# Performance work log

Measured on AMD Instinct MI355X. Metric: run time of the kernel, lower is better.

The kernel has to match this reference:

```python
import jax, jax.numpy as jnp
import numpy as np

S, H, A = 16384, 1024, 1024


def setup_inputs() -> dict:
    key = jax.random.key(0)
    k1, k2, k3, k4, k5, k6 = jax.random.split(key, 6)
    enc_out = jax.random.normal(k1, (S, 1, H), dtype=jnp.float32)
    dec_h = jax.random.normal(k2, (1, H), dtype=jnp.float32)
    mask = jax.random.randint(k3, (S, 1), 0, 2) == 1  # bool [S,1]
    # learned params (torch Linear stores weight as [out, in]; y = x @ W.T)
    W2_dec = jax.random.normal(k4, (A, H), dtype=jnp.float32) * 0.02
    W1_enc = jax.random.normal(k5, (A, H), dtype=jnp.float32) * 0.02
    V = jax.random.normal(k6, (1, A), dtype=jnp.float32) * 0.02
    return {"enc_out": enc_out, "dec_h": dec_h, "mask": mask,
            "W2_dec": W2_dec, "W1_enc": W1_enc, "V": V}


def reference(enc_out, dec_h, mask, W2_dec, W1_enc, V):
    enc = jnp.squeeze(enc_out, axis=1)            # [S, H]
    d = dec_h @ W2_dec.T                          # [1, A]
    e = enc @ W1_enc.T                            # [S, A]
    u = jnp.tanh(d + e) @ V.T                     # [S, 1]
    u = jnp.where(mask, -jnp.inf, u)              # masked logits (returned, like in-place fill)
    a = jax.nn.softmax(u, axis=0)                 # softmax over seq dim
    out = jnp.sum(a * enc, axis=0)                # [H]
    return (out, u)
```

## Files before the change

### kernel.cpp

```cpp
#include <hip/hip_runtime.h>
#include <math.h>
#include <stdint.h>

#define S_DIM 16384
#define H_DIM 1024
#define A_DIM 1024

#define MASK_NEG (-3.0e38f)

typedef __attribute__((ext_vector_type(8))) _Float16 f16x8;
typedef __attribute__((ext_vector_type(4))) float f32x4;
typedef __attribute__((address_space(3))) uint32_t as3_u32;
typedef __attribute__((address_space(1))) uint32_t as1_u32;

__device__ __forceinline__ float fast_tanh(float x) {
    float e = __expf(2.0f * x);
    return 1.0f - 2.0f * __builtin_amdgcn_rcpf(e + 1.0f);
}


__global__ __launch_bounds__(256) void prep_kernel(
        const float* __restrict__ W1, _Float16* __restrict__ W1_h,
        const float* __restrict__ dec_h, const float* __restrict__ W2,
        float* __restrict__ d, float* __restrict__ u_acc,
        const void* __restrict__ mask, int* __restrict__ mflag) {
    const int b = blockIdx.x;
    const int t = threadIdx.x;
    if (b < 64) {
        const int tb = b >> 4, kt = b & 15;
        uint4* dchunk = (uint4*)W1_h + (size_t)(tb * 16 + kt) * 1024;
        const float* srow = W1 + (size_t)tb * 256 * H_DIM + kt * 32;
        #pragma unroll
        for (int it = 0; it < 4; ++it) {
            const int idx  = it * 256 + t;
            const int r    = idx >> 2;
            const int slot = idx & 3;
            const int cg   = (slot + (r >> 1)) & 3;
            const float* sp = srow + (size_t)r * H_DIM + cg * 8;
            float4 v0 = ((const float4*)sp)[0];
            float4 v1 = ((const float4*)sp)[1];
            union { _Float16 h[8]; uint4 u; } pk;
            pk.h[0] = (_Float16)v0.x; pk.h[1] = (_Float16)v0.y;
            pk.h[2] = (_Float16)v0.z; pk.h[3] = (_Float16)v0.w;
            pk.h[4] = (_Float16)v1.x; pk.h[5] = (_Float16)v1.y;
            pk.h[6] = (_Float16)v1.z; pk.h[7] = (_Float16)v1.w;
            dchunk[idx] = pk.u;
        }
        u_acc[b * 256 + t] = 0.0f;
    } else if (b < 1088) {
        const int a = b - 64;
        const float* row = W2 + (size_t)a * H_DIM;
        float s = 0.0f;
        for (int h = t; h < H_DIM; h += 256) s += dec_h[h] * row[h];
        #pragma unroll
        for (int off = 32; off; off >>= 1) s += __shfl_down(s, off, 64);
        __shared__ float wsum[4];
        if ((t & 63) == 0) wsum[t >> 6] = s;
        __syncthreads();
        if (t == 0) d[a] = wsum[0] + wsum[1] + wsum[2] + wsum[3];
    } else {
        const unsigned char* mb = (const unsigned char*)mask;
        unsigned int orv = 0;
        for (int i = t; i < S_DIM; i += 256)
            if (i & 3) orv |= mb[i];
        __shared__ int oflag;
        if (t == 0) oflag = 0;
        __syncthreads();
        if (orv) oflag = 1;
        __syncthreads();
        if (t == 0) mflag[0] = oflag;
    }
}

__global__ __launch_bounds__(512, 1) void fused_gemm_f16_2ph(
        const float* __restrict__ enc,
        const _Float16* __restrict__ Bg,
        const float* __restrict__ V,
        const float* __restrict__ d,
        float* __restrict__ u_acc) {
    __shared__ __align__(16) _Float16 AB[2][32768];

    const int tid  = threadIdx.x;
    const int wave = tid >> 6;
    const int lane = tid & 63;
    const int quad = lane >> 4;
    const int l16  = lane & 15;
    const int wm   = wave >> 2;
    const int wn   = wave & 3;
    const int s0   = blockIdx.x * 256;
    const int a0   = blockIdx.y * 256;

    const int rowoff = (wave & 3) * 64;
    const int lrow  = lane >> 2;
    const int slotc = lane & 3;
    const int cg    = (slotc + (lrow >> 1)) & 3;

    const float* asrc[4];
    #pragma unroll
    for (int j = 0; j < 4; ++j)
        asrc[j] = enc + (size_t)(s0 + rowoff + j * 16 + lrow) * H_DIM + cg * 8;
    const _Float16* gtile = Bg + (size_t)blockIdx.y * (16 * 8192) + rowoff * 32 + lane * 8;
    _Float16* lbaseB = &AB[0][8192 + rowoff * 32];

    const int sw = ((quad - (l16 >> 1)) & 3) * 8;
    int aoff[8], boff[4];
    #pragma unroll
    for (int mi = 0; mi < 8; ++mi)
        aoff[mi] = (wm * 128 + mi * 16 + l16) * 32 + sw;
    #pragma unroll
    for (int ni = 0; ni < 4; ++ni)
        boff[ni] = 8192 + (wn * 64 + ni * 16 + l16) * 32 + sw;

    f32x4 acc[8][4];
    #pragma unroll
    for (int mi = 0; mi < 8; ++mi)
        #pragma unroll
        for (int ni = 0; ni < 4; ++ni)
            acc[mi][ni] = (f32x4){0.f, 0.f, 0.f, 0.f};

    const _Float16* hAB = &AB[0][0];

    auto pack8 = [](float4 a, float4 b) -> uint4 {
        union { _Float16 h[8]; uint4 u; } pk;
        pk.h[0] = (_Float16)a.x; pk.h[1] = (_Float16)a.y;
        pk.h[2] = (_Float16)a.z; pk.h[3] = (_Float16)a.w;
        pk.h[4] = (_Float16)b.x; pk.h[5] = (_Float16)b.y;
        pk.h[6] = (_Float16)b.z; pk.h[7] = (_Float16)b.w;
        return pk.u;
    };
    auto STAGE_A = [&](int buf, int s, int kt) {
        #pragma unroll
        for (int j = 0; j < 4; ++j) {
            float4 x0 = *(const float4*)(asrc[j] + kt * 32);
            float4 x1 = *(const float4*)(asrc[j] + kt * 32 + 4);
            *(uint4*)&AB[buf][s * 16384 + rowoff * 32 + j * 512 + lane * 8] = pack8(x0, x1);
        }
    };
    auto COMPUTE = [&](int base) {
        f16x8 bf[4];
        #pragma unroll
        for (int ni = 0; ni < 4; ++ni)
            bf[ni] = *(const f16x8*)&hAB[base + boff[ni]];
        #pragma unroll
        for (int mi = 0; mi < 8; ++mi) {
            f16x8 af = *(const f16x8*)&hAB[base + aoff[mi]];
            #pragma unroll
            for (int ni = 0; ni < 4; ++ni)
                acc[mi][ni] = __builtin_amdgcn_mfma_f32_16x16x32_f16(af, bf[ni], acc[mi][ni], 0, 0, 0);
        }
    };

    if (wave < 4) {
        STAGE_A(0, 0, 0);
        STAGE_A(0, 1, 1);
        asm volatile("s_waitcnt lgkmcnt(0)" ::: "memory");
    } else {
        #pragma unroll
        for (int s = 0; s < 2; ++s)
            #pragma unroll
            for (int j = 0; j < 4; ++j)
                __builtin_amdgcn_global_load_lds(
                    (const as1_u32*)(const void*)(gtile + s * 8192 + j * 512),
                    (as3_u32*)(void*)(lbaseB + s * 16384 + j * 512), 16, 0, 0);
    }

    for (int ph = 0; ph < 16; ++ph) {
        const int b = ph & 1;
        if (wave >= 4) {
            if (ph < 15) {
                #pragma unroll
                for (int s = 0; s < 2; ++s)
                    #pragma unroll
                    for (int j = 0; j < 4; ++j)
                        __builtin_amdgcn_global_load_lds(
                            (const as1_u32*)(const void*)(gtile + (size_t)((ph + 1) * 2 + s) * 8192 + j * 512),
                            (as3_u32*)(void*)(lbaseB + (b ^ 1) * 32768 + s * 16384 + j * 512),
                            16, 0, 0);
                asm volatile("s_waitcnt vmcnt(8)" ::: "memory");
            } else {
                asm volatile("s_waitcnt vmcnt(0)" ::: "memory");
            }
        }
        __builtin_amdgcn_sched_barrier(0);
        __builtin_amdgcn_s_barrier();
        __builtin_amdgcn_sched_barrier(0);

        if (ph < 15 && wave < 4)
            STAGE_A(b ^ 1, 0, (ph + 1) * 2);

        __builtin_amdgcn_s_setprio(1);
        COMPUTE(b * 32768);
        __builtin_amdgcn_s_setprio(0);

        if (ph < 15 && wave < 4)
            STAGE_A(b ^ 1, 1, (ph + 1) * 2 + 1);

        __builtin_amdgcn_s_setprio(1);
        COMPUTE(b * 32768 + 16384);
        __builtin_amdgcn_s_setprio(0);

        if (ph < 15) {
            if (wave < 4)
                asm volatile("s_waitcnt lgkmcnt(0)" ::: "memory");
            __builtin_amdgcn_sched_barrier(0);
            __builtin_amdgcn_s_barrier();
            __builtin_amdgcn_sched_barrier(0);
        }
    }

    float* P = (float*)&AB[0][0];
    float vv[4], dd[4];
    #pragma unroll
    for (int ni = 0; ni < 4; ++ni) {
        int c = a0 + wn * 64 + ni * 16 + l16;
        vv[ni] = V[c];
        dd[ni] = d[c];
    }
    #pragma unroll
    for (int mi = 0; mi < 8; ++mi) {
        #pragma unroll
        for (int reg = 0; reg < 4; ++reg) {
            float s = 0.0f;
            #pragma unroll
            for (int ni = 0; ni < 4; ++ni)
                s += vv[ni] * fast_tanh(dd[ni] + acc[mi][ni][reg]);
            #pragma unroll
            for (int off = 1; off < 16; off <<= 1)
                s += __shfl_xor(s, off, 64);
            if (l16 == 0)
                P[(wm * 128 + mi * 16 + quad * 4 + reg) * 4 + wn] = s;
        }
    }
    __syncthreads();
    if (tid < 256)
        atomicAdd(u_acc + s0 + tid,
                  P[tid * 4 + 0] + P[tid * 4 + 1] + P[tid * 4 + 2] + P[tid * 4 + 3]);
}

__global__ __launch_bounds__(256) void fused_gemm(const float* __restrict__ enc,
                                                  const float* __restrict__ W1,
                                                  const float* __restrict__ V,
                                                  const float* __restrict__ d,
                                                  float* __restrict__ u_acc) {
    __shared__ __align__(16) float As[16][128 + 4];
    __shared__ __align__(16) float Bs[16][128 + 4];
    const int tid = threadIdx.x;
    const int tx = tid & 15, ty = tid >> 4;
    const int s0 = blockIdx.y * 128, a0 = blockIdx.x * 128;
    const int lr = tid >> 2, lc = tid & 3;
    float acc[8][8] = {};
    for (int kt = 0; kt < H_DIM / 16; ++kt) {
        const int k0 = kt * 16;
        float4 av0 = *(const float4*)(enc + (size_t)(s0 + lr)      * H_DIM + k0 + 4 * lc);
        float4 av1 = *(const float4*)(enc + (size_t)(s0 + lr + 64) * H_DIM + k0 + 4 * lc);
        float4 bv0 = *(const float4*)(W1  + (size_t)(a0 + lr)      * H_DIM + k0 + 4 * lc);
        float4 bv1 = *(const float4*)(W1  + (size_t)(a0 + lr + 64) * H_DIM + k0 + 4 * lc);
        __syncthreads();
        As[4*lc+0][lr] = av0.x; As[4*lc+1][lr] = av0.y; As[4*lc+2][lr] = av0.z; As[4*lc+3][lr] = av0.w;
        As[4*lc+0][lr+64] = av1.x; As[4*lc+1][lr+64] = av1.y; As[4*lc+2][lr+64] = av1.z; As[4*lc+3][lr+64] = av1.w;
        Bs[4*lc+0][lr] = bv0.x; Bs[4*lc+1][lr] = bv0.y; Bs[4*lc+2][lr] = bv0.z; Bs[4*lc+3][lr] = bv0.w;
        Bs[4*lc+0][lr+64] = bv1.x; Bs[4*lc+1][lr+64] = bv1.y; Bs[4*lc+2][lr+64] = bv1.z; Bs[4*lc+3][lr+64] = bv1.w;
        __syncthreads();
        #pragma unroll
        for (int k = 0; k < 16; ++k) {
            float4 A0 = *(const float4*)&As[k][8 * ty];
            float4 A1 = *(const float4*)&As[k][8 * ty + 4];
            float4 B0 = *(const float4*)&Bs[k][8 * tx];
            float4 B1 = *(const float4*)&Bs[k][8 * tx + 4];
            float ar[8] = {A0.x, A0.y, A0.z, A0.w, A1.x, A1.y, A1.z, A1.w};
            float br[8] = {B0.x, B0.y, B0.z, B0.w, B1.x, B1.y, B1.z, B1.w};
            #pragma unroll
            for (int i = 0; i < 8; ++i)
                #pragma unroll
                for (int j = 0; j < 8; ++j)
                    acc[i][j] = fmaf(ar[i], br[j], acc[i][j]);
        }
    }
    float vv[8], dd[8];
    #pragma unroll
    for (int j = 0; j < 8; ++j) { int c = a0 + 8 * tx + j; vv[j] = V[c]; dd[j] = d[c]; }
    float pu[8];
    #pragma unroll
    for (int i = 0; i < 8; ++i) {
        float s = 0.0f;
        #pragma unroll
        for (int j = 0; j < 8; ++j) s += vv[j] * fast_tanh(dd[j] + acc[i][j]);
        pu[i] = s;
    }
    __syncthreads();
    float* Pf = &As[0][0];
    #pragma unroll
    for (int i = 0; i < 8; ++i) Pf[(8 * ty + i) * 16 + tx] = pu[i];
    __syncthreads();
    if (tid < 128) {
        float s = 0.0f;
        #pragma unroll
        for (int j = 0; j < 16; ++j) s += Pf[tid * 16 + j];
        atomicAdd(u_acc + s0 + tid, s);
    }
}

__global__ __launch_bounds__(1024) void softmax_kernel(const float* __restrict__ u_acc,
                                                       const void* __restrict__ mask,
                                                       float* __restrict__ u_out,
                                                       float* __restrict__ p) {
    const int t = threadIdx.x;
    const unsigned char* mb = (const unsigned char*)mask;
    const int* mi = (const int*)mask;

    unsigned int orv = 0;
    for (int i = t; i < S_DIM; i += 1024)
        if (i & 3) orv |= mb[i];
    __shared__ int sflag;
    if (t == 0) sflag = 0;
    __syncthreads();
    if (orv) sflag = 1;
    __syncthreads();
    const int bytemask = sflag;

    float v[16];
    float lmax = -INFINITY;
    #pragma unroll
    for (int i = 0; i < 16; ++i) {
        int r = t + i * 1024;
        int m = bytemask ? (int)mb[r] : mi[r];
        float val = m ? MASK_NEG : u_acc[r];
        u_out[r] = val;
        v[i] = val;
        lmax = fmaxf(lmax, val);
    }

    __shared__ float red[16];
    __shared__ float sm, sdenom;
    #pragma unroll
    for (int off = 32; off; off >>= 1) lmax = fmaxf(lmax, __shfl_down(lmax, off, 64));
    int wid = t >> 6, lane = t & 63;
    if (lane == 0) red[wid] = lmax;
    __syncthreads();
    if (t == 0) {
        float m2 = -INFINITY;
        for (int i = 0; i < 16; ++i) m2 = fmaxf(m2, red[i]);
        sm = m2;
    }
    __syncthreads();
    const float m = sm;

    float lsum = 0.0f;
    #pragma unroll
    for (int i = 0; i < 16; ++i) {
        v[i] = expf(v[i] - m);
        lsum += v[i];
    }
    #pragma unroll
    for (int off = 32; off; off >>= 1) lsum += __shfl_down(lsum, off, 64);
    if (lane == 0) red[wid] = lsum;
    __syncthreads();
    if (t == 0) {
        float s2 = 0.0f;
        for (int i = 0; i < 16; ++i) s2 += red[i];
        sdenom = s2;
    }
    __syncthreads();
    const float inv = 1.0f / sdenom;
    #pragma unroll
    for (int i = 0; i < 16; ++i) p[t + i * 1024] = v[i] * inv;
}

__global__ __launch_bounds__(256) void tail_part(
        const float* __restrict__ enc,
        const float* __restrict__ u_acc,
        const void* __restrict__ mask,
        const int* __restrict__ mflag,
        float* __restrict__ u_out,
        float* __restrict__ part,
        float* __restrict__ pm,
        float* __restrict__ pd) {
    const int t = threadIdx.x;
    const int b = blockIdx.x;
    const int s0 = b * 32;
    __shared__ float wsh[32];

    if (t < 32) {
        const int s = s0 + t;
        int msk = mflag[0] ? (int)((const unsigned char*)mask)[s]
                           : ((const int*)mask)[s];
        float val = msk ? MASK_NEG : u_acc[s];
        u_out[s] = val;
        float m_b = val;
        #pragma unroll
        for (int off = 16; off; off >>= 1)
            m_b = fmaxf(m_b, __shfl_xor(m_b, off, 64));
        float w = msk ? 0.0f : expf(val - m_b);
        wsh[t] = w;
        float D = w;
        #pragma unroll
        for (int off = 16; off; off >>= 1)
            D += __shfl_xor(D, off, 64);
        if (t == 0) { pm[b] = m_b; pd[b] = D; }
    }
    __syncthreads();

    const float4* encv = (const float4*)enc;
    float4 acc = {0.f, 0.f, 0.f, 0.f};
    for (int i = 0; i < 32; ++i) {
        float w = wsh[i];
        if (w != 0.0f) {
            float4 e = encv[(size_t)(s0 + i) * 256 + t];
            acc.x += w * e.x;
            acc.y += w * e.y;
            acc.z += w * e.z;
            acc.w += w * e.w;
        }
    }
    ((float4*)(part + (size_t)b * 1024))[t] = acc;
}

__global__ __launch_bounds__(256) void tail_reduce(
        const float* __restrict__ part, const float* __restrict__ pm,
        const float* __restrict__ pd, float* __restrict__ out) {
    __shared__ float scale[512];
    __shared__ float red[256];
    __shared__ float ginv;
    const int t = threadIdx.x;

    red[t] = fmaxf(pm[t], pm[t + 256]);
    __syncthreads();
    #pragma unroll
    for (int off = 128; off; off >>= 1) {
        if (t < off) red[t] = fmaxf(red[t], red[t + off]);
        __syncthreads();
    }
    const float gm = red[0];
    __syncthreads();

    float sc0 = expf(pm[t] - gm);
    float sc1 = expf(pm[t + 256] - gm);
    scale[t] = sc0; scale[t + 256] = sc1;
    red[t] = sc0 * pd[t] + sc1 * pd[t + 256];
    __syncthreads();
    #pragma unroll
    for (int off = 128; off; off >>= 1) {
        if (t < off) red[t] += red[t + off];
        __syncthreads();
    }
    if (t == 0) ginv = 1.0f / red[0];
    __syncthreads();

    const int col = blockIdx.x * 16 + (t & 15);
    const int seg = t >> 4;
    float s = 0.0f;
    for (int b2 = seg * 32; b2 < seg * 32 + 32; ++b2)
        s += scale[b2] * part[(size_t)b2 * 1024 + col];
    red[t] = s;
    __syncthreads();
    if (t < 16) {
        float r = 0.0f;
        #pragma unroll
        for (int k = 0; k < 16; ++k) r += red[k * 16 + t];
        out[col] = r * ginv;
    }
}

__global__ __launch_bounds__(256) void weighted_sum(const float* __restrict__ enc,
                                                    const float* __restrict__ p,
                                                    float* __restrict__ out) {
    const int t = threadIdx.x;
    const int s0 = blockIdx.x * 32;
    const float4* encv = (const float4*)enc;
    float4 acc = {0.0f, 0.0f, 0.0f, 0.0f};
    for (int s = s0; s < s0 + 32; ++s) {
        float ps = p[s];
        float4 e = encv[(size_t)s * 256 + t];
        acc.x += ps * e.x; acc.y += ps * e.y; acc.z += ps * e.z; acc.w += ps * e.w;
    }
    atomicAdd(out + 4 * t + 0, acc.x);
    atomicAdd(out + 4 * t + 1, acc.y);
    atomicAdd(out + 4 * t + 2, acc.z);
    atomicAdd(out + 4 * t + 3, acc.w);
}
__global__ void zero_kernel(float* __restrict__ u_acc, float* __restrict__ out) {
    int i = blockIdx.x * 256 + threadIdx.x;
    if (i < S_DIM) u_acc[i] = 0.0f;
    if (i < H_DIM) out[i]   = 0.0f;
}
__global__ __launch_bounds__(256) void dec_proj(const float* __restrict__ dec_h,
                                                const float* __restrict__ W2,
                                                float* __restrict__ d) {
    int a = blockIdx.x;
    int t = threadIdx.x;
    const float* row = W2 + (size_t)a * H_DIM;
    float s = 0.0f;
    for (int h = t; h < H_DIM; h += 256) s += dec_h[h] * row[h];
    #pragma unroll
    for (int off = 32; off; off >>= 1) s += __shfl_down(s, off, 64);
    __shared__ float wsum[4];
    if ((t & 63) == 0) wsum[t >> 6] = s;
    __syncthreads();
    if (t == 0) d[a] = wsum[0] + wsum[1] + wsum[2] + wsum[3];
}

extern "C" void kernel_launch(void* const* d_in, const int* in_sizes, int n_in,
                              void* d_out, int out_size, void* d_ws, size_t ws_size,
                              hipStream_t stream) {
    const float* enc   = (const float*)d_in[0];
    const float* dec_h = (const float*)d_in[1];
    const void*  mask  = d_in[2];
    const float* W2    = (const float*)d_in[3];
    const float* W1    = (const float*)d_in[4];
    const float* V     = (const float*)d_in[5];

    float* out   = (float*)d_out;
    float* u_out = (float*)d_out + H_DIM;

    float* ws    = (float*)d_ws;
    float* d     = ws;
    float* u_acc = ws + A_DIM;
    float* p     = ws + A_DIM + S_DIM;
    float* pm    = p;
    float* pd    = p + 512;
    int*   mflag = (int*)(p + 1024);
    float* part  = ws + A_DIM + 2 * S_DIM;
    size_t f_end = (size_t)(A_DIM + 2 * S_DIM + 512 * 1024);
    _Float16* W1_h = (_Float16*)(ws + f_end);
    size_t need_bytes = f_end * 4 + (size_t)A_DIM * H_DIM * 2;

    int dev = 0;
    hipGetDevice(&dev);
    int max_lds = 0;
    hipDeviceGetAttribute(&max_lds, hipDeviceAttributeMaxSharedMemoryPerBlock, dev);

    if (ws_size >= need_bytes && max_lds >= 131072) {
        prep_kernel<<<1089, 256, 0, stream>>>(W1, W1_h, dec_h, W2,
                                              d, u_acc, mask, mflag);
        fused_gemm_f16_2ph<<<dim3(S_DIM / 256, A_DIM / 256), 512, 0, stream>>>(
            enc, W1_h, V, d, u_acc);
        tail_part<<<S_DIM / 32, 256, 0, stream>>>(enc, u_acc, mask, mflag,
                                                  u_out, part, pm, pd);
        tail_reduce<<<64, 256, 0, stream>>>(part, pm, pd, out);
    } else {
        zero_kernel<<<64, 256, 0, stream>>>(u_acc, out);
        dec_proj<<<A_DIM, 256, 0, stream>>>(dec_h, W2, d);
        fused_gemm<<<dim3(A_DIM / 128, S_DIM / 128), 256, 0, stream>>>(enc, W1, V, d, u_acc);
        softmax_kernel<<<1, 1024, 0, stream>>>(u_acc, mask, u_out, p);
        weighted_sum<<<S_DIM / 32, 256, 0, stream>>>(enc, p, out);
    }
}
```

Baseline: 182.1 us.

## Convert W1 to f16 inside GEMM staging and drop prep-time pre-conversion

Removes the prep-kernel pass that converted W1 to a swizzled f16 copy in workspace. The GEMM now has all 8 waves stage both A (enc) and B (W1) tiles from fp32 global memory, converting to f16 on the fly, instead of splitting waves into enc converters and async global_load_lds loaders. This drops a 4MB read and 2MB write in prep, but each GEMM block now reads fp32 W1 (twice the bytes) and does more conversion work. It also loses the async direct-to-LDS path for B.

```diff
diff --git a/kernel.cpp b/kernel.cpp
--- a/kernel.cpp
+++ b/kernel.cpp
@@ -20,32 +20,12 @@
 
 
 __global__ __launch_bounds__(256) void prep_kernel(
-        const float* __restrict__ W1, _Float16* __restrict__ W1_h,
         const float* __restrict__ dec_h, const float* __restrict__ W2,
         float* __restrict__ d, float* __restrict__ u_acc,
         const void* __restrict__ mask, int* __restrict__ mflag) {
     const int b = blockIdx.x;
     const int t = threadIdx.x;
     if (b < 64) {
-        const int tb = b >> 4, kt = b & 15;
-        uint4* dchunk = (uint4*)W1_h + (size_t)(tb * 16 + kt) * 1024;
-        const float* srow = W1 + (size_t)tb * 256 * H_DIM + kt * 32;
-        #pragma unroll
-        for (int it = 0; it < 4; ++it) {
-            const int idx  = it * 256 + t;
-            const int r    = idx >> 2;
-            const int slot = idx & 3;
-            const int cg   = (slot + (r >> 1)) & 3;
-            const float* sp = srow + (size_t)r * H_DIM + cg * 8;
-            float4 v0 = ((const float4*)sp)[0];
-            float4 v1 = ((const float4*)sp)[1];
-            union { _Float16 h[8]; uint4 u; } pk;
-            pk.h[0] = (_Float16)v0.x; pk.h[1] = (_Float16)v0.y;
-            pk.h[2] = (_Float16)v0.z; pk.h[3] = (_Float16)v0.w;
-            pk.h[4] = (_Float16)v1.x; pk.h[5] = (_Float16)v1.y;
-            pk.h[6] = (_Float16)v1.z; pk.h[7] = (_Float16)v1.w;
-            dchunk[idx] = pk.u;
-        }
         u_acc[b * 256 + t] = 0.0f;
     } else if (b < 1088) {
         const int a = b - 64;
@@ -74,7 +54,7 @@
 
 __global__ __launch_bounds__(512, 1) void fused_gemm_f16_2ph(
         const float* __restrict__ enc,
-        const _Float16* __restrict__ Bg,
+        const float* __restrict__ W1,
         const float* __restrict__ V,
         const float* __restrict__ d,
         float* __restrict__ u_acc) {
@@ -90,17 +70,10 @@
     const int s0   = blockIdx.x * 256;
     const int a0   = blockIdx.y * 256;
 
-    const int rowoff = (wave & 3) * 64;
-    const int lrow  = lane >> 2;
-    const int slotc = lane & 3;
-    const int cg    = (slotc + (lrow >> 1)) & 3;
-
-    const float* asrc[4];
-    #pragma unroll
-    for (int j = 0; j < 4; ++j)
-        asrc[j] = enc + (size_t)(s0 + rowoff + j * 16 + lrow) * H_DIM + cg * 8;
-    const _Float16* gtile = Bg + (size_t)blockIdx.y * (16 * 8192) + rowoff * 32 + lane * 8;
-    _Float16* lbaseB = &AB[0][8192 + rowoff * 32];
+    const int rS = wave * 32 + (lane >> 1);
+    const int c0 = (lane & 1) * 2;
+    const float* aRow = enc + (size_t)(s0 + rS) * H_DIM;
+    const float* bRow = W1  + (size_t)(a0 + rS) * H_DIM;
 
     const int sw = ((quad - (l16 >> 1)) & 3) * 8;
     int aoff[8], boff[4];
@@ -128,12 +101,20 @@
         pk.h[6] = (_Float16)b.z; pk.h[7] = (_Float16)b.w;
         return pk.u;
     };
-    auto STAGE_A = [&](int buf, int s, int kt) {
-        #pragma unroll
-        for (int j = 0; j < 4; ++j) {
-            float4 x0 = *(const float4*)(asrc[j] + kt * 32);
-            float4 x1 = *(const float4*)(asrc[j] + kt * 32 + 4);
-            *(uint4*)&AB[buf][s * 16384 + rowoff * 32 + j * 512 + lane * 8] = pack8(x0, x1);
+    auto STAGE = [&](int buf, int s, int kt) {
+        const int base = buf * 32768 + s * 16384;
+        #pragma unroll
+        for (int u = 0; u < 2; ++u) {
+            const int c  = c0 + u;
+            const int cg = (c + (rS >> 1)) & 3;
+            const float* pa = aRow + kt * 32 + cg * 8;
+            float4 xa0 = ((const float4*)pa)[0];
+            float4 xa1 = ((const float4*)pa)[1];
+            *(uint4*)&AB[0][base + rS * 32 + c * 8] = pack8(xa0, xa1);
+            const float* pb = bRow + kt * 32 + cg * 8;
+            float4 xb0 = ((const float4*)pb)[0];
+            float4 xb1 = ((const float4*)pb)[1];
+            *(uint4*)&AB[0][base + 8192 + rS * 32 + c * 8] = pack8(xb0, xb1);
         }
     };
     auto COMPUTE = [&](int base) {
@@ -150,58 +131,31 @@
         }
     };
 
-    if (wave < 4) {
-        STAGE_A(0, 0, 0);
-        STAGE_A(0, 1, 1);
-        asm volatile("s_waitcnt lgkmcnt(0)" ::: "memory");
-    } else {
-        #pragma unroll
-        for (int s = 0; s < 2; ++s)
-            #pragma unroll
-            for (int j = 0; j < 4; ++j)
-                __builtin_amdgcn_global_load_lds(
-                    (const as1_u32*)(const void*)(gtile + s * 8192 + j * 512),
-                    (as3_u32*)(void*)(lbaseB + s * 16384 + j * 512), 16, 0, 0);
-    }
+    STAGE(0, 0, 0);
+    STAGE(0, 1, 1);
+    asm volatile("s_waitcnt lgkmcnt(0)" ::: "memory");
+    __builtin_amdgcn_sched_barrier(0);
+    __builtin_amdgcn_s_barrier();
+    __builtin_amdgcn_sched_barrier(0);
 
     for (int ph = 0; ph < 16; ++ph) {
         const int b = ph & 1;
-        if (wave >= 4) {
-            if (ph < 15) {
-                #pragma unroll
-                for (int s = 0; s < 2; ++s)
-                    #pragma unroll
-                    for (int j = 0; j < 4; ++j)
-                        __builtin_amdgcn_global_load_lds(
-                            (const as1_u32*)(const void*)(gtile + (size_t)((ph + 1) * 2 + s) * 8192 + j * 512),
-                            (as3_u32*)(void*)(lbaseB + (b ^ 1) * 32768 + s * 16384 + j * 512),
-                            16, 0, 0);
-                asm volatile("s_waitcnt vmcnt(8)" ::: "memory");
-            } else {
-                asm volatile("s_waitcnt vmcnt(0)" ::: "memory");
-            }
-        }
-        __builtin_amdgcn_sched_barrier(0);
-        __builtin_amdgcn_s_barrier();
-        __builtin_amdgcn_sched_barrier(0);
-
-        if (ph < 15 && wave < 4)
-            STAGE_A(b ^ 1, 0, (ph + 1) * 2);
+        if (ph < 15)
+            STAGE(b ^ 1, 0, (ph + 1) * 2);
 
         __builtin_amdgcn_s_setprio(1);
         COMPUTE(b * 32768);
         __builtin_amdgcn_s_setprio(0);
 
-        if (ph < 15 && wave < 4)
-            STAGE_A(b ^ 1, 1, (ph + 1) * 2 + 1);
+        if (ph < 15)
+            STAGE(b ^ 1, 1, (ph + 1) * 2 + 1);
 
         __builtin_amdgcn_s_setprio(1);
         COMPUTE(b * 32768 + 16384);
         __builtin_amdgcn_s_setprio(0);
 
         if (ph < 15) {
-            if (wave < 4)
-                asm volatile("s_waitcnt lgkmcnt(0)" ::: "memory");
+            asm volatile("s_waitcnt lgkmcnt(0)" ::: "memory");
             __builtin_amdgcn_sched_barrier(0);
             __builtin_amdgcn_s_barrier();
             __builtin_amdgcn_sched_barrier(0);
@@ -521,8 +475,7 @@
     int*   mflag = (int*)(p + 1024);
     float* part  = ws + A_DIM + 2 * S_DIM;
     size_t f_end = (size_t)(A_DIM + 2 * S_DIM + 512 * 1024);
-    _Float16* W1_h = (_Float16*)(ws + f_end);
-    size_t need_bytes = f_end * 4 + (size_t)A_DIM * H_DIM * 2;
+    size_t need_bytes = f_end * 4;
 
     int dev = 0;
     hipGetDevice(&dev);
@@ -530,10 +483,9 @@
     hipDeviceGetAttribute(&max_lds, hipDeviceAttributeMaxSharedMemoryPerBlock, dev);
 
     if (ws_size >= need_bytes && max_lds >= 131072) {
-        prep_kernel<<<1089, 256, 0, stream>>>(W1, W1_h, dec_h, W2,
-                                              d, u_acc, mask, mflag);
+        prep_kernel<<<1089, 256, 0, stream>>>(dec_h, W2, d, u_acc, mask, mflag);
         fused_gemm_f16_2ph<<<dim3(S_DIM / 256, A_DIM / 256), 512, 0, stream>>>(
-            enc, W1_h, V, d, u_acc);
+            enc, W1, V, d, u_acc);
         tail_part<<<S_DIM / 32, 256, 0, stream>>>(enc, u_acc, mask, mflag,
                                                   u_out, part, pm, pd);
         tail_reduce<<<64, 256, 0, stream>>>(part, pm, pd, out);
```

After: 197.2 us. 1.08x slower.
